# Kernel tuning notes

Hardware: AMD Instinct MI355X
Metric: run time of the kernel (lower is better)

Reference implementation:

```python
import jax, jax.numpy as jnp
import numpy as np

B, TQ, TK, D = 16, 2048, 2048, 128


def setup_inputs() -> dict:
    key = jax.random.key(0)
    kq, kk, kv, km = jax.random.split(key, 4)
    query = jax.random.normal(kq, (B, TQ, D), dtype=jnp.float32)
    key_t = jax.random.normal(kk, (B, TK, D), dtype=jnp.float32)
    value = jax.random.normal(kv, (B, TK, D), dtype=jnp.float32)
    mask = (jax.random.uniform(km, (B, TQ, TK)) > 0.9).astype(jnp.float32)
    return {"query": query, "key": key_t, "value": value, "mask": mask}


def reference(query, key, value, mask):
    # score = Q K^T / sqrt(dk)
    dk = jnp.asarray(query.shape[-1], query.dtype)
    score = jnp.einsum("bqd,bkd->bqk", query, key) / jnp.sqrt(dk)
    score = score + mask * (-10000.0)
    # NOTE: original code applies softmax over axis=1 (the query axis),
    # not the usual last axis; reproduced faithfully.
    attn_weights = jax.nn.softmax(score, axis=1)
    context = jnp.einsum("bqk,bkv->bqv", attn_weights, value)
    return context, attn_weights
```

## Files before the change

kernel.cpp:

```cpp
#include <hip/hip_runtime.h>

typedef __attribute__((ext_vector_type(8))) short s8v;
typedef __attribute__((ext_vector_type(4))) float f4v;

constexpr int BN = 16;
constexpr int TQ = 2048;
constexpr int TK = 2048;
constexpr int DH = 128;

__device__ __forceinline__ unsigned short f2bf(float f) {
  unsigned int u = __float_as_uint(f);
  u += 0x7fffu + ((u >> 16) & 1u);
  return (unsigned short)(u >> 16);
}
__device__ __forceinline__ float bf2f(unsigned short h) {
  return __uint_as_float(((unsigned int)h) << 16);
}

__global__ __launch_bounds__(256) void qk_exp_kernel(
    const float* __restrict__ Q, const float* __restrict__ K,
    const float* __restrict__ Msk, float* __restrict__ P,
    float* __restrict__ Z)
{
  __shared__ __align__(16) unsigned short qhi[128][40];
  __shared__ __align__(16) unsigned short qlo[128][40];
  __shared__ __align__(16) unsigned short khi[128][40];
  __shared__ __align__(16) unsigned short klo[128][40];

  const int kb = blockIdx.x, qb = blockIdx.y, b = blockIdx.z;
  const int tid = threadIdx.x;
  const int wave = tid >> 6, lane = tid & 63;
  const int wr = wave >> 1, wc = wave & 1;
  const int quad = lane >> 4, l16 = lane & 15;

  f4v acc[4][4];
#pragma unroll
  for (int i = 0; i < 4; ++i)
#pragma unroll
    for (int j = 0; j < 4; ++j)
      acc[i][j] = (f4v){0.f, 0.f, 0.f, 0.f};

  const float* Qb = Q + ((size_t)b * TQ + (size_t)qb * 128) * DH;
  const float* Kb = K + ((size_t)b * TK + (size_t)kb * 128) * DH;

  for (int dc = 0; dc < DH; dc += 32) {
    __syncthreads();
#pragma unroll
    for (int i = 0; i < 4; ++i) {
      int idx = i * 256 + tid;
      int r = idx >> 3, c = (idx & 7) * 4;
      float4 qv = *(const float4*)(Qb + (size_t)r * DH + dc + c);
      float4 kv = *(const float4*)(Kb + (size_t)r * DH + dc + c);
      unsigned short h;
      h = f2bf(qv.x); qhi[r][c+0] = h; qlo[r][c+0] = f2bf(qv.x - bf2f(h));
      h = f2bf(qv.y); qhi[r][c+1] = h; qlo[r][c+1] = f2bf(qv.y - bf2f(h));
      h = f2bf(qv.z); qhi[r][c+2] = h; qlo[r][c+2] = f2bf(qv.z - bf2f(h));
      h = f2bf(qv.w); qhi[r][c+3] = h; qlo[r][c+3] = f2bf(qv.w - bf2f(h));
      h = f2bf(kv.x); khi[r][c+0] = h; klo[r][c+0] = f2bf(kv.x - bf2f(h));
      h = f2bf(kv.y); khi[r][c+1] = h; klo[r][c+1] = f2bf(kv.y - bf2f(h));
      h = f2bf(kv.z); khi[r][c+2] = h; klo[r][c+2] = f2bf(kv.z - bf2f(h));
      h = f2bf(kv.w); khi[r][c+3] = h; klo[r][c+3] = f2bf(kv.w - bf2f(h));
    }
    __syncthreads();

    s8v ah[4], al[4], bh[4], bl[4];
#pragma unroll
    for (int i = 0; i < 4; ++i) {
      ah[i] = *(const s8v*)&qhi[wr*64 + i*16 + l16][quad*8];
      al[i] = *(const s8v*)&qlo[wr*64 + i*16 + l16][quad*8];
      bh[i] = *(const s8v*)&khi[wc*64 + i*16 + l16][quad*8];
      bl[i] = *(const s8v*)&klo[wc*64 + i*16 + l16][quad*8];
    }
#pragma unroll
    for (int i = 0; i < 4; ++i)
#pragma unroll
      for (int j = 0; j < 4; ++j) {
        acc[i][j] = __builtin_amdgcn_mfma_f32_16x16x32_bf16(ah[i], bh[j], acc[i][j], 0, 0, 0);
        acc[i][j] = __builtin_amdgcn_mfma_f32_16x16x32_bf16(al[i], bh[j], acc[i][j], 0, 0, 0);
        acc[i][j] = __builtin_amdgcn_mfma_f32_16x16x32_bf16(ah[i], bl[j], acc[i][j], 0, 0, 0);
      }
  }

  const float scale = 0.08838834764831845f;
  float csum[4] = {0.f, 0.f, 0.f, 0.f};
#pragma unroll
  for (int j = 0; j < 4; ++j) {
    int col = kb * 128 + wc * 64 + j * 16 + l16;
#pragma unroll
    for (int i = 0; i < 4; ++i) {
      int row0 = qb * 128 + wr * 64 + i * 16 + quad * 4;
#pragma unroll
      for (int r = 0; r < 4; ++r) {
        size_t off = ((size_t)b * TQ + row0 + r) * TK + col;
        float s = acc[i][j][r] * scale - 10000.0f * Msk[off];
        float p = __expf(s);
        P[off] = p;
        csum[j] += p;
      }
    }
  }
#pragma unroll
  for (int j = 0; j < 4; ++j) {
    float v = csum[j];
    v += __shfl_xor(v, 16, 64);
    v += __shfl_xor(v, 32, 64);
    if (quad == 0)
      atomicAdd(&Z[b * TK + kb * 128 + wc * 64 + j * 16 + l16], v);
  }
}

__global__ __launch_bounds__(256) void vtrans_kernel(
    const float* __restrict__ V, unsigned short* __restrict__ Vthi,
    unsigned short* __restrict__ Vtlo)
{
  __shared__ float tile[64][65];
  const int k0 = blockIdx.x * 64, d0 = blockIdx.y * 64, b = blockIdx.z;
  const int tid = threadIdx.x;
#pragma unroll
  for (int i = 0; i < 4; ++i) {
    int idx = i * 256 + tid;
    int r = idx >> 4, c = (idx & 15) * 4;
    float4 v = *(const float4*)(V + ((size_t)b * TK + k0 + r) * DH + d0 + c);
    tile[r][c] = v.x; tile[r][c+1] = v.y; tile[r][c+2] = v.z; tile[r][c+3] = v.w;
  }
  __syncthreads();
  const int dr = tid >> 2, kq = (tid & 3) * 16;
  size_t base = ((size_t)b * DH + d0 + dr) * TK + k0 + kq;
  unsigned short hbuf[16], lbuf[16];
#pragma unroll
  for (int j = 0; j < 16; ++j) {
    float f = tile[kq + j][dr];
    unsigned short h = f2bf(f);
    hbuf[j] = h;
    lbuf[j] = f2bf(f - bf2f(h));
  }
#pragma unroll
  for (int m = 0; m < 4; ++m) {
    ushort4 hv = make_ushort4(hbuf[4*m], hbuf[4*m+1], hbuf[4*m+2], hbuf[4*m+3]);
    ushort4 lv = make_ushort4(lbuf[4*m], lbuf[4*m+1], lbuf[4*m+2], lbuf[4*m+3]);
    *(ushort4*)(Vthi + base + 4*m) = hv;
    *(ushort4*)(Vtlo + base + 4*m) = lv;
  }
}

__global__ __launch_bounds__(256) void rz_kernel(const float* __restrict__ Z,
                                                 float* __restrict__ Rz) {
  int i = blockIdx.x * 256 + threadIdx.x;
  Rz[i] = 1.0f / Z[i];
}

union __align__(16) AVSH {
  struct {
    unsigned short a[64][40];
    unsigned short vh[128][40];
    unsigned short vl[128][40];
  } b[2];
  float ctx[64][131];
};

__global__ __launch_bounds__(256) void av_kernel(
    float* __restrict__ Attn, const unsigned short* __restrict__ Vthi,
    const unsigned short* __restrict__ Vtlo, const float* __restrict__ Rz,
    float* __restrict__ Ctx)
{
  __shared__ AVSH sh;
  const int qb = blockIdx.x, b = blockIdx.y;
  const int tid = threadIdx.x;
  const int wave = tid >> 6, lane = tid & 63;
  const int wr = wave >> 1, wc = wave & 1;
  const int quad = lane >> 4, l16 = lane & 15;

  f4v acc[4][2];
#pragma unroll
  for (int i = 0; i < 4; ++i)
#pragma unroll
    for (int j = 0; j < 2; ++j)
      acc[i][j] = (f4v){0.f, 0.f, 0.f, 0.f};

  float* attnB = Attn + ((size_t)b * TQ + (size_t)qb * 64) * TK;
  const unsigned short* vhB = Vthi + (size_t)b * DH * TK;
  const unsigned short* vlB = Vtlo + (size_t)b * DH * TK;
  const float* rzB = Rz + (size_t)b * TK;

  const int pc = (tid & 7) * 4;
  const int pr = tid >> 3;
  const int vc = (tid & 3) * 8;
  const int vr = tid >> 2;

  float4 pv0, pv1, rzv;
  uint4 vh0, vh1, vl0, vl1;

  auto load_chunk = [&](int kc) {
    pv0 = *(const float4*)(attnB + (size_t)pr * TK + kc + pc);
    pv1 = *(const float4*)(attnB + (size_t)(pr + 32) * TK + kc + pc);
    rzv = *(const float4*)(rzB + kc + pc);
    vh0 = *(const uint4*)(vhB + (size_t)vr * TK + kc + vc);
    vh1 = *(const uint4*)(vhB + (size_t)(vr + 64) * TK + kc + vc);
    vl0 = *(const uint4*)(vlB + (size_t)vr * TK + kc + vc);
    vl1 = *(const uint4*)(vlB + (size_t)(vr + 64) * TK + kc + vc);
  };

  auto stage_chunk = [&](int kc, int B) {
    float4 a0, a1;
    a0.x = pv0.x * rzv.x; a0.y = pv0.y * rzv.y;
    a0.z = pv0.z * rzv.z; a0.w = pv0.w * rzv.w;
    a1.x = pv1.x * rzv.x; a1.y = pv1.y * rzv.y;
    a1.z = pv1.z * rzv.z; a1.w = pv1.w * rzv.w;
    *(float4*)(attnB + (size_t)pr * TK + kc + pc) = a0;
    *(float4*)(attnB + (size_t)(pr + 32) * TK + kc + pc) = a1;
    *(ushort4*)&sh.b[B].a[pr][pc] =
        make_ushort4(f2bf(a0.x), f2bf(a0.y), f2bf(a0.z), f2bf(a0.w));
    *(ushort4*)&sh.b[B].a[pr + 32][pc] =
        make_ushort4(f2bf(a1.x), f2bf(a1.y), f2bf(a1.z), f2bf(a1.w));
    *(uint4*)&sh.b[B].vh[vr][vc] = vh0;
    *(uint4*)&sh.b[B].vh[vr + 64][vc] = vh1;
    *(uint4*)&sh.b[B].vl[vr][vc] = vl0;
    *(uint4*)&sh.b[B].vl[vr + 64][vc] = vl1;
  };

  load_chunk(0);
  stage_chunk(0, 0);
  __syncthreads();

  int cur = 0;
  constexpr int NT = TK / 32;
  for (int t = 0; t < NT; ++t) {
    if (t + 1 < NT) load_chunk((t + 1) * 32);

    s8v vhf[4], vlf[4], pf[2];
#pragma unroll
    for (int i = 0; i < 4; ++i) {
      vhf[i] = *(const s8v*)&sh.b[cur].vh[wr * 64 + i * 16 + l16][quad * 8];
      vlf[i] = *(const s8v*)&sh.b[cur].vl[wr * 64 + i * 16 + l16][quad * 8];
    }
#pragma unroll
    for (int j = 0; j < 2; ++j)
      pf[j] = *(const s8v*)&sh.b[cur].a[wc * 32 + j * 16 + l16][quad * 8];

#pragma unroll
    for (int i = 0; i < 4; ++i)
#pragma unroll
      for (int j = 0; j < 2; ++j) {
        acc[i][j] = __builtin_amdgcn_mfma_f32_16x16x32_bf16(vhf[i], pf[j], acc[i][j], 0, 0, 0);
        acc[i][j] = __builtin_amdgcn_mfma_f32_16x16x32_bf16(vlf[i], pf[j], acc[i][j], 0, 0, 0);
      }

    if (t + 1 < NT) {
      stage_chunk((t + 1) * 32, cur ^ 1);
      __syncthreads();
      cur ^= 1;
    }
  }

  __syncthreads();
#pragma unroll
  for (int i = 0; i < 4; ++i)
#pragma unroll
    for (int j = 0; j < 2; ++j)
#pragma unroll
      for (int r = 0; r < 4; ++r)
        sh.ctx[wc * 32 + j * 16 + l16][wr * 64 + i * 16 + quad * 4 + r] = acc[i][j][r];
  __syncthreads();
#pragma unroll
  for (int it = 0; it < 8; ++it) {
    int idx = it * 256 + tid;
    int r = idx >> 5, c = (idx & 31) * 4;
    float4 v;
    v.x = sh.ctx[r][c];     v.y = sh.ctx[r][c + 1];
    v.z = sh.ctx[r][c + 2]; v.w = sh.ctx[r][c + 3];
    *(float4*)(Ctx + ((size_t)b * TQ + qb * 64 + r) * DH + c) = v;
  }
}

extern "C" void kernel_launch(void* const* d_in, const int* in_sizes, int n_in,
                              void* d_out, int out_size, void* d_ws, size_t ws_size,
                              hipStream_t stream)
{
  const float* Q = (const float*)d_in[0];
  const float* K = (const float*)d_in[1];
  const float* V = (const float*)d_in[2];
  const float* M = (const float*)d_in[3];

  float* ctx  = (float*)d_out;
  float* attn = ctx + (size_t)BN * TQ * DH;

  char* ws = (char*)d_ws;
  float* Z = (float*)ws;
  unsigned short* Vthi = (unsigned short*)(ws + (1 << 20));
  unsigned short* Vtlo = Vthi + (size_t)BN * DH * TK;
  float* Rz = (float*)(ws + (1 << 20) + (size_t)BN * DH * TK * 4);

  hipMemsetAsync(Z, 0, (size_t)BN * TK * sizeof(float), stream);
  vtrans_kernel<<<dim3(TK/64, DH/64, BN), 256, 0, stream>>>(V, Vthi, Vtlo);
  qk_exp_kernel<<<dim3(TK/128, TQ/128, BN), 256, 0, stream>>>(Q, K, M, attn, Z);
  rz_kernel<<<dim3((BN*TK)/256), 256, 0, stream>>>(Z, Rz);
  av_kernel<<<dim3(TQ/64, BN), 256, 0, stream>>>(attn, Vthi, Vtlo, Rz, ctx);
}
```

Baseline: 772.5 us.

## Pack the binary mask into bitfields and raise QK kernel occupancy

Adds a pre-pass kernel that reads the float mask with fully coalesced loads and packs it into one bit per element. The QK/exp kernel then reads compact mask words and writes zero for masked entries instead of loading a float mask value per output element. It also loads K fragments per column tile inside the MFMA loop to cut register pressure and requests 4 blocks per CU through launch bounds. The full float mask is still read once, so the cost is an extra kernel launch plus a small bitmask round trip. The packing assumes the mask is strictly binary.

```diff
diff --git a/kernel.cpp b/kernel.cpp
--- a/kernel.cpp
+++ b/kernel.cpp
@@ -17,9 +17,29 @@
   return __uint_as_float(((unsigned int)h) << 16);
 }
 
-__global__ __launch_bounds__(256) void qk_exp_kernel(
+__global__ __launch_bounds__(256) void maskbits_kernel(
+    const float* __restrict__ Msk, unsigned int* __restrict__ Mb)
+{
+  __shared__ unsigned char nib[256];
+  const int tid = threadIdx.x;
+  const size_t base = (size_t)blockIdx.x * 1024;
+  float4 v = *(const float4*)(Msk + base + (size_t)tid * 4);
+  unsigned char n = (v.x != 0.f ? 1u : 0u) | (v.y != 0.f ? 2u : 0u) |
+                    (v.z != 0.f ? 4u : 0u) | (v.w != 0.f ? 8u : 0u);
+  nib[tid] = n;
+  __syncthreads();
+  if (tid < 32) {
+    unsigned int w = 0;
+#pragma unroll
+    for (int j = 0; j < 8; ++j)
+      w |= (unsigned int)nib[tid * 8 + j] << (j * 4);
+    Mb[(size_t)blockIdx.x * 32 + tid] = w;
+  }
+}
+
+__global__ __launch_bounds__(256, 4) void qk_exp_kernel(
     const float* __restrict__ Q, const float* __restrict__ K,
-    const float* __restrict__ Msk, float* __restrict__ P,
+    const unsigned int* __restrict__ Mb, float* __restrict__ P,
     float* __restrict__ Z)
 {
   __shared__ __align__(16) unsigned short qhi[128][40];
@@ -63,38 +83,44 @@
     }
     __syncthreads();
 
-    s8v ah[4], al[4], bh[4], bl[4];
+    s8v ah[4], al[4];
 #pragma unroll
     for (int i = 0; i < 4; ++i) {
       ah[i] = *(const s8v*)&qhi[wr*64 + i*16 + l16][quad*8];
       al[i] = *(const s8v*)&qlo[wr*64 + i*16 + l16][quad*8];
-      bh[i] = *(const s8v*)&khi[wc*64 + i*16 + l16][quad*8];
-      bl[i] = *(const s8v*)&klo[wc*64 + i*16 + l16][quad*8];
-    }
-#pragma unroll
-    for (int i = 0; i < 4; ++i)
+    }
+#pragma unroll
+    for (int j = 0; j < 4; ++j) {
+      s8v bh = *(const s8v*)&khi[wc*64 + j*16 + l16][quad*8];
+      s8v bl = *(const s8v*)&klo[wc*64 + j*16 + l16][quad*8];
+#pragma unroll
+      for (int i = 0; i < 4; ++i) {
+        acc[i][j] = __builtin_amdgcn_mfma_f32_16x16x32_bf16(ah[i], bh, acc[i][j], 0, 0, 0);
+        acc[i][j] = __builtin_amdgcn_mfma_f32_16x16x32_bf16(al[i], bh, acc[i][j], 0, 0, 0);
+        acc[i][j] = __builtin_amdgcn_mfma_f32_16x16x32_bf16(ah[i], bl, acc[i][j], 0, 0, 0);
+      }
+    }
+  }
+
+  const float scale = 0.08838834764831845f;
+  const unsigned int* MbB = Mb + (size_t)b * TQ * (TK / 32) + kb * 4 + wc * 2;
+  float csum[4] = {0.f, 0.f, 0.f, 0.f};
+#pragma unroll
+  for (int i = 0; i < 4; ++i) {
+    int row0 = qb * 128 + wr * 64 + i * 16 + quad * 4;
+    uint2 w[4];
+#pragma unroll
+    for (int r = 0; r < 4; ++r)
+      w[r] = *(const uint2*)(MbB + (size_t)(row0 + r) * (TK / 32));
+#pragma unroll
+    for (int r = 0; r < 4; ++r) {
+      size_t rowoff = ((size_t)b * TQ + row0 + r) * TK + kb * 128 + wc * 64;
 #pragma unroll
       for (int j = 0; j < 4; ++j) {
-        acc[i][j] = __builtin_amdgcn_mfma_f32_16x16x32_bf16(ah[i], bh[j], acc[i][j], 0, 0, 0);
-        acc[i][j] = __builtin_amdgcn_mfma_f32_16x16x32_bf16(al[i], bh[j], acc[i][j], 0, 0, 0);
-        acc[i][j] = __builtin_amdgcn_mfma_f32_16x16x32_bf16(ah[i], bl[j], acc[i][j], 0, 0, 0);
-      }
-  }
-
-  const float scale = 0.08838834764831845f;
-  float csum[4] = {0.f, 0.f, 0.f, 0.f};
-#pragma unroll
-  for (int j = 0; j < 4; ++j) {
-    int col = kb * 128 + wc * 64 + j * 16 + l16;
-#pragma unroll
-    for (int i = 0; i < 4; ++i) {
-      int row0 = qb * 128 + wr * 64 + i * 16 + quad * 4;
-#pragma unroll
-      for (int r = 0; r < 4; ++r) {
-        size_t off = ((size_t)b * TQ + row0 + r) * TK + col;
-        float s = acc[i][j][r] * scale - 10000.0f * Msk[off];
-        float p = __expf(s);
-        P[off] = p;
+        unsigned int bits = (j < 2) ? w[r].x : w[r].y;
+        unsigned int m = (bits >> ((j & 1) * 16 + l16)) & 1u;
+        float p = m ? 0.f : __expf(acc[i][j][r] * scale);
+        P[rowoff + j * 16 + l16] = p;
         csum[j] += p;
       }
     }
@@ -285,14 +311,16 @@
   float* attn = ctx + (size_t)BN * TQ * DH;
 
   char* ws = (char*)d_ws;
-  float* Z = (float*)ws;
+  float* Z  = (float*)ws;
+  float* Rz = (float*)(ws + (128 << 10));
   unsigned short* Vthi = (unsigned short*)(ws + (1 << 20));
   unsigned short* Vtlo = Vthi + (size_t)BN * DH * TK;
-  float* Rz = (float*)(ws + (1 << 20) + (size_t)BN * DH * TK * 4);
+  unsigned int* Mbits = (unsigned int*)(ws + (17u << 20));
 
   hipMemsetAsync(Z, 0, (size_t)BN * TK * sizeof(float), stream);
+  maskbits_kernel<<<dim3((BN * TQ * TK) / 1024), 256, 0, stream>>>(M, Mbits);
   vtrans_kernel<<<dim3(TK/64, DH/64, BN), 256, 0, stream>>>(V, Vthi, Vtlo);
-  qk_exp_kernel<<<dim3(TK/128, TQ/128, BN), 256, 0, stream>>>(Q, K, M, attn, Z);
+  qk_exp_kernel<<<dim3(TK/128, TQ/128, BN), 256, 0, stream>>>(Q, K, Mbits, attn, Z);
   rz_kernel<<<dim3((BN*TK)/256), 256, 0, stream>>>(Z, Rz);
   av_kernel<<<dim3(TQ/64, BN), 256, 0, stream>>>(attn, Vthi, Vtlo, Rz, ctx);
 }
```

Result: faster. 742.0 us (-3.9%).
